# Kernel optimization log

Hardware: AMD Instinct MI355X
Metric: run time of the kernel (lower is better)

Reference implementation:

```python
import jax, jax.numpy as jnp
import numpy as np

B_FACTOR = 4          # branching factor of the complete tree
DEPTH = 7             # levels 0..DEPTH; level DEPTH are leaves
N_NODES = (B_FACTOR ** (DEPTH + 1) - 1) // (B_FACTOR - 1)   # 21845
N_INTERNAL = (B_FACTOR ** DEPTH - 1) // (B_FACTOR - 1)      # 5461
IN_SIZE = 512
HID = 512
PARAM_SCALE = 0.02


def setup_inputs() -> dict:
    key = jax.random.key(0)
    ks = jax.random.split(key, 7)
    x = jax.random.normal(ks[0], (N_NODES, IN_SIZE), dtype=jnp.float32)
    # torch nn.Linear parameters: y = x @ W.T + b
    W_iou = jax.random.normal(ks[1], (3 * HID, IN_SIZE), dtype=jnp.float32) * PARAM_SCALE
    b_iou = jax.random.normal(ks[2], (3 * HID,), dtype=jnp.float32) * PARAM_SCALE
    W_f = jax.random.normal(ks[3], (HID, IN_SIZE), dtype=jnp.float32) * PARAM_SCALE
    b_f = jax.random.normal(ks[4], (HID,), dtype=jnp.float32) * PARAM_SCALE
    U_iou = jax.random.normal(ks[5], (3 * HID, HID), dtype=jnp.float32) * PARAM_SCALE
    U_f = jax.random.normal(ks[6], (HID, HID), dtype=jnp.float32) * PARAM_SCALE
    # children[j] = indices of the 4 children of internal node j (complete 4-ary tree)
    children = (B_FACTOR * jnp.arange(N_INTERNAL, dtype=jnp.int32)[:, None]
                + jnp.arange(1, B_FACTOR + 1, dtype=jnp.int32)[None, :])
    return {"x": x, "children": children, "W_iou": W_iou, "b_iou": b_iou,
            "W_f": W_f, "b_f": b_f, "U_iou": U_iou, "U_f": U_f}


def reference(x, children, W_iou, b_iou, W_f, b_f, U_iou, U_f):
    """Child-Sum Tree-LSTM over a complete 4-ary tree, processed level-batched
    bottom-up (equivalent to the per-node postorder recursion in the source).
    Leaves keep h = c = 0, as in the source (_forward_postorder returns early).
    NOTE: the source applies NO sigmoid to the forget gate term; we keep that.
    """
    N = x.shape[0]
    H = U_f.shape[0]
    # input-dependent parts are tree-independent: precompute once for all nodes
    wx_iou = x @ W_iou.T + b_iou          # [N, 3H]
    wx_f = x @ W_f.T + b_f                # [N, H]
    h = jnp.zeros((N, H), dtype=x.dtype)
    c = jnp.zeros_like(h)
    # level l occupies node indices [offs[l], offs[l+1]) — static constants
    offs = [(B_FACTOR ** l - 1) // (B_FACTOR - 1) for l in range(DEPTH + 2)]
    for l in range(DEPTH - 1, -1, -1):    # internal levels, deepest first
        s, e = offs[l], offs[l + 1]
        ch = children[s:e]                # [M, 4]
        h_ch = h[ch]                      # [M, 4, H] gather of child hidden states
        c_ch = c[ch]                      # [M, 4, H]
        h_sum = h_ch.sum(axis=1)          # child-sum
        iou = wx_iou[s:e] + h_sum @ U_iou.T               # [M, 3H]
        i, o, u = jnp.split(iou, 3, axis=-1)
        i = jax.nn.sigmoid(i)
        o = jax.nn.sigmoid(o)
        u = jnp.tanh(u)
        # forget term per child (no sigmoid, faithful to source)
        f = wx_f[s:e][:, None, :] + h_ch @ U_f.T          # [M, 4, H]
        c_new = i * u + (f * c_ch).sum(axis=1)            # [M, H]
        h = h.at[s:e].set(o * jnp.tanh(c_new))
        c = c.at[s:e].set(c_new)
    return h, c
```

## Files before the change

### kernel.cpp

```cpp
#include <hip/hip_runtime.h>
#include <cmath>

constexpr int N_NODES = 21845;
constexpr int N_INT   = 5461;
constexpr int HID     = 512;

typedef short  short8  __attribute__((ext_vector_type(8)));
typedef float  floatx4 __attribute__((ext_vector_type(4)));

__device__ __forceinline__ unsigned short f2bf(float f) {
    unsigned int u = __float_as_uint(f);
    u += 0x7fffu + ((u >> 16) & 1u);
    return (unsigned short)(u >> 16);
}

__global__ void prep_kernel(const float* __restrict__ x,
                            const float* __restrict__ W_iou,
                            const float* __restrict__ W_f,
                            const float* __restrict__ U_iou,
                            const float* __restrict__ U_f,
                            float* __restrict__ h_leaf,
                            float* __restrict__ c_leaf,
                            unsigned short* __restrict__ dstb)
{
    const size_t Z  = (size_t)(N_NODES - N_INT) * HID / 4;
    const size_t C0 = (size_t)N_INT * 512 / 4;
    const size_t C1 = C0 + 1536 * 512 / 4;
    const size_t C2 = C1 + 512 * 512 / 4;
    const size_t C3 = C2 + 1536 * 512 / 4;
    const size_t C4 = C3 + 512 * 512 / 4;
    const size_t total = 2 * Z + C4;
    size_t i = (size_t)blockIdx.x * blockDim.x + threadIdx.x;
    const size_t stride = (size_t)gridDim.x * blockDim.x;
    const float4 zz = {0.f, 0.f, 0.f, 0.f};
    for (; i < total; i += stride) {
        if (i < 2 * Z) {
            if (i < Z) ((float4*)h_leaf)[i] = zz;
            else       ((float4*)c_leaf)[i - Z] = zz;
        } else {
            size_t k = i - 2 * Z;
            const float* src; size_t off;
            if (k < C0)      { src = x;     off = k; }
            else if (k < C1) { src = W_iou; off = k - C0; }
            else if (k < C2) { src = W_f;   off = k - C1; }
            else if (k < C3) { src = U_iou; off = k - C2; }
            else             { src = U_f;   off = k - C3; }
            float4 v = ((const float4*)src)[off];
            ushort4 o;
            o.x = f2bf(v.x); o.y = f2bf(v.y); o.z = f2bf(v.z); o.w = f2bf(v.w);
            ((ushort4*)dstb)[k] = o;
        }
    }
}

#define GLD_LDS(g, l) __builtin_amdgcn_global_load_lds( \
    (const __attribute__((address_space(1))) void*)(g), \
    (__attribute__((address_space(3))) void*)(l), 16, 0, 0)

__device__ __forceinline__ void gemm_tile_128(
    const unsigned short* __restrict__ A, int Arows,
    const unsigned short* __restrict__ B,
    const float* __restrict__ bias,
    float* __restrict__ C, int ldc,
    int bm, int bn)
{
    __shared__ short8 AsV[1024];
    __shared__ short8 BsV[1024];

    const int tid  = threadIdx.x;
    const int wave = tid >> 6;
    const int lane = tid & 63;
    const int quad = lane >> 4;
    const int lr   = lane & 15;
    const int wr = (wave >> 1) * 64;
    const int wc = (wave & 1) * 64;

    floatx4 acc[4][4];
    #pragma unroll
    for (int i = 0; i < 4; ++i)
        #pragma unroll
        for (int j = 0; j < 4; ++j)
            acc[i][j] = (floatx4){0.f, 0.f, 0.f, 0.f};

    int s_row[4], s_gk[4];
    #pragma unroll
    for (int it = 0; it < 4; ++it) {
        int c = it * 256 + wave * 64 + lane;
        s_row[it] = c >> 3;
        s_gk[it]  = (c & 7) ^ (s_row[it] & 7);
    }

    for (int k0 = 0; k0 < 512; k0 += 64) {
        #pragma unroll
        for (int it = 0; it < 4; ++it) {
            int row = s_row[it];
            int gm = bm + row; if (gm >= Arows) gm = Arows - 1;
            GLD_LDS(A + (size_t)gm * 512 + k0 + s_gk[it] * 8, &AsV[it * 256 + wave * 64]);
            int gn = bn + row;
            GLD_LDS(B + (size_t)gn * 512 + k0 + s_gk[it] * 8, &BsV[it * 256 + wave * 64]);
        }
        __syncthreads();

        #pragma unroll
        for (int kc = 0; kc < 2; ++kc) {
            short8 af[4], bfr[4];
            const int q = kc * 4 + quad;
            #pragma unroll
            for (int mt = 0; mt < 4; ++mt) {
                int row = wr + mt * 16 + lr;
                af[mt] = AsV[row * 8 + (q ^ (row & 7))];
            }
            #pragma unroll
            for (int nt = 0; nt < 4; ++nt) {
                int row = wc + nt * 16 + lr;
                bfr[nt] = BsV[row * 8 + (q ^ (row & 7))];
            }
            #pragma unroll
            for (int mt = 0; mt < 4; ++mt)
                #pragma unroll
                for (int nt = 0; nt < 4; ++nt)
                    acc[mt][nt] = __builtin_amdgcn_mfma_f32_16x16x32_bf16(
                        af[mt], bfr[nt], acc[mt][nt], 0, 0, 0);
        }
        __syncthreads();
    }

    #pragma unroll
    for (int mt = 0; mt < 4; ++mt) {
        #pragma unroll
        for (int r = 0; r < 4; ++r) {
            int gm = bm + wr + mt * 16 + quad * 4 + r;
            if (gm >= Arows) continue;
            #pragma unroll
            for (int nt = 0; nt < 4; ++nt) {
                int gn = bn + wc + nt * 16 + lr;
                float v = acc[mt][nt][r];
                if (bias) v += bias[gn];
                C[(size_t)gm * ldc + gn] = v;
            }
        }
    }
}

__global__ __launch_bounds__(256) void wgemm_kernel(
    const unsigned short* __restrict__ xb,
    const unsigned short* __restrict__ Wib,
    const unsigned short* __restrict__ Wfb,
    const float* __restrict__ b_iou, const float* __restrict__ b_f,
    float* __restrict__ wx_iou, float* __restrict__ wx_f)
{
    int b = blockIdx.x;
    if (b < 516) {
        gemm_tile_128(xb, N_INT, Wib, b_iou, wx_iou, 1536, (b / 12) * 128, (b % 12) * 128);
    } else {
        int b2 = b - 516;
        gemm_tile_128(xb, 1365, Wfb, b_f, wx_f, 512, (b2 / 4) * 128, (b2 % 4) * 128);
    }
}

__global__ __launch_bounds__(512) void combine6_kernel(
    const float* __restrict__ wx_iou,
    float* __restrict__ h_out, float* __restrict__ c_out,
    unsigned short* __restrict__ h_bf, unsigned short* __restrict__ hs_out)
{
    __shared__ float4 hsbuf[512];
    const int k  = threadIdx.x >> 7;
    const int jg = threadIdx.x & 127;
    const int j4 = jg << 2;

    for (int tp = blockIdx.x; tp < 1024; tp += gridDim.x) {
        const int n = 1365 + 4 * tp + k;
        const float* wrow = wx_iou + (size_t)n * 1536 + j4;
        float4 iv = *(const float4*)(wrow);
        float4 ov = *(const float4*)(wrow + 512);
        float4 uv = *(const float4*)(wrow + 1024);
        float4 cn, hn; ushort4 hb;
        #pragma unroll
        for (int c = 0; c < 4; ++c) {
            float ig = 1.f / (1.f + expf(-((float*)&iv)[c]));
            float og = 1.f / (1.f + expf(-((float*)&ov)[c]));
            float ug = tanhf(((float*)&uv)[c]);
            float cv2 = ig * ug;
            float hv = og * tanhf(cv2);
            ((float*)&cn)[c] = cv2;
            ((float*)&hn)[c] = hv;
            ((unsigned short*)&hb)[c] = f2bf(hv);
        }
        *(float4*)(c_out + (size_t)n * 512 + j4) = cn;
        *(float4*)(h_out + (size_t)n * 512 + j4) = hn;
        *(ushort4*)(h_bf + (size_t)n * 512 + j4) = hb;
        hsbuf[threadIdx.x] = hn;
        __syncthreads();
        if (threadIdx.x < 128) {
            float4 s0 = hsbuf[jg], s1 = hsbuf[128 + jg], s2 = hsbuf[256 + jg], s3 = hsbuf[384 + jg];
            ushort4 ho;
            #pragma unroll
            for (int c = 0; c < 4; ++c)
                ((unsigned short*)&ho)[c] =
                    f2bf(((float*)&s0)[c] + ((float*)&s1)[c] + ((float*)&s2)[c] + ((float*)&s3)[c]);
            *(ushort4*)(hs_out + (size_t)tp * 512 + j4) = ho;
        }
        __syncthreads();
    }
}

__device__ __forceinline__ void dtile(
    const unsigned short* __restrict__ A, int Arows,
    const unsigned short* __restrict__ B, int brow0,
    float* __restrict__ lds_out, int ldl, int col0, int rows_store)
{
    const int lane = threadIdx.x & 63;
    const int quad = lane >> 4;
    const int lr   = lane & 15;
    const int ar   = lr < Arows ? lr : Arows - 1;
    const unsigned short* ap = A + (size_t)ar * 512 + quad * 8;
    const unsigned short* bp = B + (size_t)(brow0 + lr) * 512 + quad * 8;

    floatx4 acc[4];
    #pragma unroll
    for (int j = 0; j < 4; ++j) acc[j] = (floatx4){0.f, 0.f, 0.f, 0.f};

    short8 a0 = *(const short8*)ap;
    short8 b0[4];
    #pragma unroll
    for (int j = 0; j < 4; ++j) b0[j] = *(const short8*)(bp + (size_t)j * 16 * 512);

    #pragma unroll
    for (int k = 32; k <= 512; k += 32) {
        short8 a1 = a0;
        short8 b1[4];
        #pragma unroll
        for (int j = 0; j < 4; ++j) b1[j] = b0[j];
        if (k < 512) {
            a1 = *(const short8*)(ap + k);
            #pragma unroll
            for (int j = 0; j < 4; ++j) b1[j] = *(const short8*)(bp + (size_t)j * 16 * 512 + k);
        }
        #pragma unroll
        for (int j = 0; j < 4; ++j)
            acc[j] = __builtin_amdgcn_mfma_f32_16x16x32_bf16(a0, b1[j] , acc[j], 0, 0, 0);
        #pragma unroll
        for (int j = 0; j < 4; ++j) b0[j] = b1[j];
        a0 = a1;
    }

    #pragma unroll
    for (int j = 0; j < 4; ++j) {
        #pragma unroll
        for (int r = 0; r < 4; ++r) {
            int m = quad * 4 + r;
            if (m < rows_store) lds_out[m * ldl + col0 + j * 16 + lr] = acc[j][r];
        }
    }
}

__device__ __forceinline__ void dtile2(
    const unsigned short* __restrict__ A, int Arows,
    const unsigned short* __restrict__ B, int brow0,
    float* __restrict__ lds_out, int ldl, int col0, int rows_store)
{
    const int lane = threadIdx.x & 63;
    const int quad = lane >> 4;
    const int lr   = lane & 15;
    const int ar   = lr < Arows ? lr : Arows - 1;
    const unsigned short* ap = A + (size_t)ar * 512 + quad * 8;
    const unsigned short* bp = B + (size_t)(brow0 + lr) * 512 + quad * 8;

    floatx4 acc[4];
    #pragma unroll
    for (int j = 0; j < 4; ++j) acc[j] = (floatx4){0.f, 0.f, 0.f, 0.f};

    short8 a0 = *(const short8*)ap;
    short8 b0[4];
    #pragma unroll
    for (int j = 0; j < 4; ++j) b0[j] = *(const short8*)(bp + (size_t)j * 16 * 512);

    #pragma unroll
    for (int k = 32; k <= 512; k += 32) {
        short8 a1 = a0;
        short8 b1[4];
        #pragma unroll
        for (int j = 0; j < 4; ++j) b1[j] = b0[j];
        if (k < 512) {
            a1 = *(const short8*)(ap + k);
            #pragma unroll
            for (int j = 0; j < 4; ++j) b1[j] = *(const short8*)(bp + (size_t)j * 16 * 512 + k);
        }
        #pragma unroll
        for (int j = 0; j < 4; ++j)
            acc[j] = __builtin_amdgcn_mfma_f32_16x16x32_bf16(a0, b0[j], acc[j], 0, 0, 0);
        a0 = a1;
        #pragma unroll
        for (int j = 0; j < 4; ++j) b0[j] = b1[j];
    }

    #pragma unroll
    for (int j = 0; j < 4; ++j) {
        #pragma unroll
        for (int r = 0; r < 4; ++r) {
            int m = quad * 4 + r;
            if (m < rows_store) lds_out[m * ldl + col0 + j * 16 + lr] = acc[j][r];
        }
    }
}

__global__ __launch_bounds__(512, 2) void fused_level_kernel(
    const float* __restrict__ wx_iou, const float* __restrict__ wx_f,
    const unsigned short* __restrict__ Uib, const unsigned short* __restrict__ Ufb,
    const unsigned short* __restrict__ hs_in,
    const unsigned short* __restrict__ hch,
    const float* __restrict__ c_child,
    float* __restrict__ h_out, float* __restrict__ c_out,
    unsigned short* __restrict__ h_bf,
    unsigned short* __restrict__ hs_out,
    int s, int nl)
{
    __shared__ float iou_res[4][384];
    __shared__ float f_res[16][128];
    __shared__ float hsbuf[512];

    const int bp = blockIdx.x >> 2;
    const int cs = (blockIdx.x & 3) << 7;
    const int wave = threadIdx.x >> 6;
    const int rowsA = nl < 4 ? nl : 4;
    const int rowsC = 4 * nl < 16 ? 4 * nl : 16;

    if (wave < 6) {
        const int g  = wave >> 1;
        const int lo = (wave & 1) << 6;
        dtile2(hs_in + (size_t)(4 * bp) * 512, rowsA,
               Uib, g * 512 + cs + lo,
               &iou_res[0][0], 384, g * 128 + lo, rowsA);
    } else {
        const int lo = (wave - 6) << 6;
        dtile2(hch + (size_t)(16 * bp) * 512, rowsC,
               Ufb, cs + lo,
               &f_res[0][0], 128, lo, 16);
    }
    __syncthreads();

    const int k  = threadIdx.x >> 7;
    const int jg = threadIdx.x & 127;
    const int col = cs + jg;
    float hn = 0.f;
    if (k < nl) {
        const int t = 4 * bp + k;
        const int n = s + t;
        float iv = wx_iou[(size_t)n * 1536 + col]        + iou_res[k][jg];
        float ov = wx_iou[(size_t)n * 1536 + 512 + col]  + iou_res[k][128 + jg];
        float uv = wx_iou[(size_t)n * 1536 + 1024 + col] + iou_res[k][256 + jg];
        float wf = wx_f[(size_t)n * 512 + col];
        float fc = 0.f;
        #pragma unroll
        for (int q = 0; q < 4; ++q)
            fc += (wf + f_res[4 * k + q][jg]) *
                  c_child[(size_t)(16 * bp + 4 * k + q) * 512 + col];
        float ig = 1.f / (1.f + expf(-iv));
        float og = 1.f / (1.f + expf(-ov));
        float ug = tanhf(uv);
        float cn = ig * ug + fc;
        hn = og * tanhf(cn);
        c_out[(size_t)n * 512 + col] = cn;
        h_out[(size_t)n * 512 + col] = hn;
        h_bf[(size_t)n * 512 + col] = f2bf(hn);
    }
    hsbuf[threadIdx.x] = hn;
    __syncthreads();
    if (hs_out && threadIdx.x < 128) {
        float ssum = hsbuf[jg] + hsbuf[128 + jg] + hsbuf[256 + jg] + hsbuf[384 + jg];
        hs_out[(size_t)bp * 512 + col] = f2bf(ssum);
    }
}

extern "C" void kernel_launch(void* const* d_in, const int* in_sizes, int n_in,
                              void* d_out, int out_size, void* d_ws, size_t ws_size,
                              hipStream_t stream) {
    const float* x     = (const float*)d_in[0];
    const float* W_iou = (const float*)d_in[2];
    const float* b_iou = (const float*)d_in[3];
    const float* W_f   = (const float*)d_in[4];
    const float* b_f   = (const float*)d_in[5];
    const float* U_iou = (const float*)d_in[6];
    const float* U_f   = (const float*)d_in[7];

    float* h_out = (float*)d_out;
    float* c_out = h_out + (size_t)N_NODES * HID;

    float* ws     = (float*)d_ws;
    float* wx_iou = ws;
    float* wx_f   = wx_iou + (size_t)N_INT * 1536;
    unsigned short* xb   = (unsigned short*)(wx_f + (size_t)1365 * 512);
    unsigned short* Wib  = xb  + (size_t)N_INT * 512;
    unsigned short* Wfb  = Wib + (size_t)1536 * 512;
    unsigned short* Uib  = Wfb + (size_t)512 * 512;
    unsigned short* Ufb  = Uib + (size_t)1536 * 512;
    unsigned short* h_bf = Ufb + (size_t)512 * 512;
    unsigned short* hsA  = h_bf + (size_t)N_INT * 512;
    unsigned short* hsB  = hsA  + (size_t)1024 * 512;

    const int offs[9] = {0, 1, 5, 21, 85, 341, 1365, 5461, 21845};

    prep_kernel<<<2048, 256, 0, stream>>>(x, W_iou, W_f, U_iou, U_f,
                                          h_out + (size_t)N_INT * HID,
                                          c_out + (size_t)N_INT * HID, xb);

    wgemm_kernel<<<516 + 44, 256, 0, stream>>>(xb, Wib, Wfb, b_iou, b_f, wx_iou, wx_f);

    combine6_kernel<<<1024, 512, 0, stream>>>(wx_iou, h_out, c_out, h_bf, hsA);

    unsigned short* hp[2] = {hsA, hsB};
    int pi = 0;
    for (int l = 5; l >= 0; --l) {
        const int s  = offs[l];
        const int nl = offs[l + 1] - s;
        const int np = (nl + 3) >> 2;
        fused_level_kernel<<<4 * np, 512, 0, stream>>>(
            wx_iou, wx_f, Uib, Ufb,
            hp[pi], h_bf + (size_t)offs[l + 1] * HID,
            c_out + (size_t)offs[l + 1] * HID,
            h_out, c_out, h_bf,
            (l > 0) ? hp[1 - pi] : nullptr,
            s, nl);
        pi = 1 - pi;
    }
}
```

Baseline: 342.1 us.

## Handle level 5 with wide tiled GEMMs plus separate combine kernel

Level 5 (1024 nodes) no longer goes through the per-level fused kernel with tiny 16-row MFMA tiles. It is computed with 128x128 tiled GEMMs for the U_iou child-sum and U_f per-child products, followed by a vectorized combine kernel that applies the gates and writes the child-sum for the next level. The remaining levels use a new dtile3 that preloads the whole A row into registers and double-buffers B, and the fused kernel drops its min-2-blocks launch bound. The cost is extra workspace, an extra global round trip for the GEMM outputs, and higher register pressure.

```diff
diff --git a/kernel.cpp b/kernel.cpp
--- a/kernel.cpp
+++ b/kernel.cpp
@@ -158,6 +158,21 @@
     }
 }
 
+__global__ __launch_bounds__(256) void gemm5_kernel(
+    const unsigned short* __restrict__ hs_bf,
+    const unsigned short* __restrict__ h6_bf,
+    const unsigned short* __restrict__ Uib, const unsigned short* __restrict__ Ufb,
+    float* __restrict__ ioud, float* __restrict__ fd)
+{
+    int b = blockIdx.x;
+    if (b < 96) {
+        gemm_tile_128(hs_bf, 1024, Uib, nullptr, ioud, 1536, (b / 12) * 128, (b % 12) * 128);
+    } else {
+        int b2 = b - 96;
+        gemm_tile_128(h6_bf, 4096, Ufb, nullptr, fd, 512, (b2 / 4) * 128, (b2 % 4) * 128);
+    }
+}
+
 __global__ __launch_bounds__(512) void combine6_kernel(
     const float* __restrict__ wx_iou,
     float* __restrict__ h_out, float* __restrict__ c_out,
@@ -204,7 +219,77 @@
     }
 }
 
-__device__ __forceinline__ void dtile(
+__global__ __launch_bounds__(512) void combine_wide_kernel(
+    const float* __restrict__ wx_iou, const float* __restrict__ wx_f,
+    const float* __restrict__ ioud, const float* __restrict__ fd,
+    const float* __restrict__ c_child,
+    float* __restrict__ h_out, float* __restrict__ c_out,
+    unsigned short* __restrict__ h_bf, unsigned short* __restrict__ hs_bf,
+    int s, int np)
+{
+    __shared__ float4 hsbuf[512];
+    const int k  = threadIdx.x >> 7;
+    const int jg = threadIdx.x & 127;
+    const int j4 = jg << 2;
+
+    for (int tp = blockIdx.x; tp < np; tp += gridDim.x) {
+        const int t = 4 * tp + k;
+        const int n = s + t;
+        const float* wrow = wx_iou + (size_t)n * 1536 + j4;
+        float4 iv = *(const float4*)(wrow);
+        float4 ov = *(const float4*)(wrow + 512);
+        float4 uv = *(const float4*)(wrow + 1024);
+        const float* drow = ioud + (size_t)t * 1536 + j4;
+        float4 a  = *(const float4*)(drow);
+        float4 b  = *(const float4*)(drow + 512);
+        float4 u2 = *(const float4*)(drow + 1024);
+        float4 wf = *(const float4*)(wx_f + (size_t)n * 512 + j4);
+        float4 fc = {0.f, 0.f, 0.f, 0.f};
+        #pragma unroll
+        for (int c = 0; c < 4; ++c) {
+            ((float*)&iv)[c] += ((float*)&a)[c];
+            ((float*)&ov)[c] += ((float*)&b)[c];
+            ((float*)&uv)[c] += ((float*)&u2)[c];
+        }
+        #pragma unroll
+        for (int q = 0; q < 4; ++q) {
+            float4 f  = *(const float4*)(fd + (size_t)(4 * t + q) * 512 + j4);
+            float4 cv = *(const float4*)(c_child + (size_t)(4 * t + q) * 512 + j4);
+            #pragma unroll
+            for (int c = 0; c < 4; ++c)
+                ((float*)&fc)[c] += (((float*)&wf)[c] + ((float*)&f)[c]) * ((float*)&cv)[c];
+        }
+        float4 cn, hn; ushort4 hb;
+        #pragma unroll
+        for (int c = 0; c < 4; ++c) {
+            float ig = 1.f / (1.f + expf(-((float*)&iv)[c]));
+            float og = 1.f / (1.f + expf(-((float*)&ov)[c]));
+            float ug = tanhf(((float*)&uv)[c]);
+            float cv2 = ig * ug + ((float*)&fc)[c];
+            float hv = og * tanhf(cv2);
+            ((float*)&cn)[c] = cv2;
+            ((float*)&hn)[c] = hv;
+            ((unsigned short*)&hb)[c] = f2bf(hv);
+        }
+        *(float4*)(c_out + (size_t)n * 512 + j4) = cn;
+        *(float4*)(h_out + (size_t)n * 512 + j4) = hn;
+        *(ushort4*)(h_bf + (size_t)n * 512 + j4) = hb;
+        hsbuf[threadIdx.x] = hn;
+        __syncthreads();
+        if (threadIdx.x < 128) {
+            float4 s0 = hsbuf[jg], s1 = hsbuf[128 + jg], s2 = hsbuf[256 + jg], s3 = hsbuf[384 + jg];
+            ushort4 ho;
+            #pragma unroll
+            for (int c = 0; c < 4; ++c)
+                ((unsigned short*)&ho)[c] =
+                    f2bf(((float*)&s0)[c] + ((float*)&s1)[c] + ((float*)&s2)[c] + ((float*)&s3)[c]);
+            *(ushort4*)(hs_bf + (size_t)tp * 512 + j4) = ho;
+        }
+        __syncthreads();
+    }
+}
+
+__device__ __forceinline__ void dtile3(
     const unsigned short* __restrict__ A, int Arows,
     const unsigned short* __restrict__ B, int brow0,
     float* __restrict__ lds_out, int ldl, int col0, int rows_store)
@@ -216,32 +301,29 @@
     const unsigned short* ap = A + (size_t)ar * 512 + quad * 8;
     const unsigned short* bp = B + (size_t)(brow0 + lr) * 512 + quad * 8;
 
+    short8 a[16];
+    #pragma unroll
+    for (int k = 0; k < 16; ++k) a[k] = *(const short8*)(ap + 32 * k);
+
     floatx4 acc[4];
     #pragma unroll
     for (int j = 0; j < 4; ++j) acc[j] = (floatx4){0.f, 0.f, 0.f, 0.f};
 
-    short8 a0 = *(const short8*)ap;
-    short8 b0[4];
-    #pragma unroll
-    for (int j = 0; j < 4; ++j) b0[j] = *(const short8*)(bp + (size_t)j * 16 * 512);
-
-    #pragma unroll
-    for (int k = 32; k <= 512; k += 32) {
-        short8 a1 = a0;
-        short8 b1[4];
-        #pragma unroll
-        for (int j = 0; j < 4; ++j) b1[j] = b0[j];
-        if (k < 512) {
-            a1 = *(const short8*)(ap + k);
-            #pragma unroll
-            for (int j = 0; j < 4; ++j) b1[j] = *(const short8*)(bp + (size_t)j * 16 * 512 + k);
+    short8 b[2][4];
+    #pragma unroll
+    for (int j = 0; j < 4; ++j) b[0][j] = *(const short8*)(bp + (size_t)j * 16 * 512);
+
+    #pragma unroll
+    for (int ks = 0; ks < 16; ++ks) {
+        const int cur = ks & 1, nxt = cur ^ 1;
+        if (ks < 15) {
+            #pragma unroll
+            for (int j = 0; j < 4; ++j)
+                b[nxt][j] = *(const short8*)(bp + (size_t)j * 16 * 512 + 32 * (ks + 1));
         }
         #pragma unroll
         for (int j = 0; j < 4; ++j)
-            acc[j] = __builtin_amdgcn_mfma_f32_16x16x32_bf16(a0, b1[j] , acc[j], 0, 0, 0);
-        #pragma unroll
-        for (int j = 0; j < 4; ++j) b0[j] = b1[j];
-        a0 = a1;
+            acc[j] = __builtin_amdgcn_mfma_f32_16x16x32_bf16(a[ks], b[cur][j], acc[j], 0, 0, 0);
     }
 
     #pragma unroll
@@ -254,57 +336,7 @@
     }
 }
 
-__device__ __forceinline__ void dtile2(
-    const unsigned short* __restrict__ A, int Arows,
-    const unsigned short* __restrict__ B, int brow0,
-    float* __restrict__ lds_out, int ldl, int col0, int rows_store)
-{
-    const int lane = threadIdx.x & 63;
-    const int quad = lane >> 4;
-    const int lr   = lane & 15;
-    const int ar   = lr < Arows ? lr : Arows - 1;
-    const unsigned short* ap = A + (size_t)ar * 512 + quad * 8;
-    const unsigned short* bp = B + (size_t)(brow0 + lr) * 512 + quad * 8;
-
-    floatx4 acc[4];
-    #pragma unroll
-    for (int j = 0; j < 4; ++j) acc[j] = (floatx4){0.f, 0.f, 0.f, 0.f};
-
-    short8 a0 = *(const short8*)ap;
-    short8 b0[4];
-    #pragma unroll
-    for (int j = 0; j < 4; ++j) b0[j] = *(const short8*)(bp + (size_t)j * 16 * 512);
-
-    #pragma unroll
-    for (int k = 32; k <= 512; k += 32) {
-        short8 a1 = a0;
-        short8 b1[4];
-        #pragma unroll
-        for (int j = 0; j < 4; ++j) b1[j] = b0[j];
-        if (k < 512) {
-            a1 = *(const short8*)(ap + k);
-            #pragma unroll
-            for (int j = 0; j < 4; ++j) b1[j] = *(const short8*)(bp + (size_t)j * 16 * 512 + k);
-        }
-        #pragma unroll
-        for (int j = 0; j < 4; ++j)
-            acc[j] = __builtin_amdgcn_mfma_f32_16x16x32_bf16(a0, b0[j], acc[j], 0, 0, 0);
-        a0 = a1;
-        #pragma unroll
-        for (int j = 0; j < 4; ++j) b0[j] = b1[j];
-    }
-
-    #pragma unroll
-    for (int j = 0; j < 4; ++j) {
-        #pragma unroll
-        for (int r = 0; r < 4; ++r) {
-            int m = quad * 4 + r;
-            if (m < rows_store) lds_out[m * ldl + col0 + j * 16 + lr] = acc[j][r];
-        }
-    }
-}
-
-__global__ __launch_bounds__(512, 2) void fused_level_kernel(
+__global__ __launch_bounds__(512) void fused_level_kernel(
     const float* __restrict__ wx_iou, const float* __restrict__ wx_f,
     const unsigned short* __restrict__ Uib, const unsigned short* __restrict__ Ufb,
     const unsigned short* __restrict__ hs_in,
@@ -328,12 +360,12 @@
     if (wave < 6) {
         const int g  = wave >> 1;
         const int lo = (wave & 1) << 6;
-        dtile2(hs_in + (size_t)(4 * bp) * 512, rowsA,
+        dtile3(hs_in + (size_t)(4 * bp) * 512, rowsA,
                Uib, g * 512 + cs + lo,
                &iou_res[0][0], 384, g * 128 + lo, rowsA);
     } else {
         const int lo = (wave - 6) << 6;
-        dtile2(hch + (size_t)(16 * bp) * 512, rowsC,
+        dtile3(hch + (size_t)(16 * bp) * 512, rowsC,
                Ufb, cs + lo,
                &f_res[0][0], 128, lo, 16);
     }
@@ -389,7 +421,9 @@
     float* ws     = (float*)d_ws;
     float* wx_iou = ws;
     float* wx_f   = wx_iou + (size_t)N_INT * 1536;
-    unsigned short* xb   = (unsigned short*)(wx_f + (size_t)1365 * 512);
+    float* ioud   = wx_f   + (size_t)1365 * 512;
+    float* fd     = ioud   + (size_t)1024 * 1536;
+    unsigned short* xb   = (unsigned short*)(fd + (size_t)4096 * 512);
     unsigned short* Wib  = xb  + (size_t)N_INT * 512;
     unsigned short* Wfb  = Wib + (size_t)1536 * 512;
     unsigned short* Uib  = Wfb + (size_t)512 * 512;
@@ -408,9 +442,14 @@
 
     combine6_kernel<<<1024, 512, 0, stream>>>(wx_iou, h_out, c_out, h_bf, hsA);
 
-    unsigned short* hp[2] = {hsA, hsB};
+    gemm5_kernel<<<224, 256, 0, stream>>>(hsA, h_bf + (size_t)1365 * HID, Uib, Ufb, ioud, fd);
+    combine_wide_kernel<<<256, 512, 0, stream>>>(
+        wx_iou, wx_f, ioud, fd, c_out + (size_t)1365 * HID,
+        h_out, c_out, h_bf, hsB, 341, 256);
+
+    unsigned short* hp[2] = {hsB, hsA};
     int pi = 0;
-    for (int l = 5; l >= 0; --l) {
+    for (int l = 4; l >= 0; --l) {
         const int s  = offs[l];
         const int nl = offs[l + 1] - s;
         const int np = (nl + 3) >> 2;
```

Result: faster. 294.8 us (-13.8%).
